# Kernel tuning notes

Measured on AMD Instinct MI355X. Metric: run time of the kernel, lower is better.

Reference implementation:

```python
import jax, jax.numpy as jnp
import numpy as np

B, N, F, H, F_ = 4, 2048, 64, 4, 64


def setup_inputs() -> dict:
    key = jax.random.key(0)
    kx, ka, kw, ks, kn = jax.random.split(key, 5)
    X = jax.random.normal(kx, (B, N, F), dtype=jnp.float32)
    A = (jax.random.uniform(ka, (B, N, N)) < 0.05).astype(jnp.float32)
    A = jnp.maximum(A, jnp.eye(N, dtype=jnp.float32)[None])
    W = jax.random.normal(kw, (H, F, F_), dtype=jnp.float32) * 0.1
    a_self = jax.random.normal(ks, (H, F_), dtype=jnp.float32) * 0.1
    a_neigh = jax.random.normal(kn, (H, F_), dtype=jnp.float32) * 0.1
    return {"X": X, "A": A, "W": W, "a_self": a_self, "a_neigh": a_neigh}


def reference(X, A, W, a_self, a_neigh):
    # linear transform per head: [B,H,N,F_]
    lin = jnp.einsum('bnf,hfo->bhno', X, W)
    # additive attention scores
    s_self = jnp.einsum('bhno,ho->bhn', lin, a_self)[:, :, :, None]   # [B,H,N,1]
    s_neigh = jnp.einsum('bhno,ho->bhn', lin, a_neigh)[:, :, None, :]  # [B,H,1,N]
    dense = s_self + s_neigh                                           # [B,H,N,N]
    dense = jnp.where(dense >= 0, dense, 0.2 * dense)                  # LeakyReLU(0.2)
    BIG = jnp.float32(1e10)
    mask = jnp.exp(A * -BIG) * -BIG                                    # 0 where edge, -1e10 where no edge
    logits = dense + mask[:, None, :, :]
    attn = jax.nn.softmax(logits, axis=-1)
    # dropout is identity at inference (attn_dropout=0.0)
    feats = jnp.einsum('bhnm,bhmo->bhno', attn, lin)                   # [B,H,N,F_]
    feats = jax.nn.relu(feats)                                         # activation before concat
    b, h, n, f_ = feats.shape
    out = feats.transpose(0, 2, 1, 3).reshape(b, n, h * f_)            # concat heads
    return out
```

## Files before the change

### kernel.cpp

```cpp
#include <hip/hip_runtime.h>

#define BB 4
#define NN 2048
#define FF 64
#define HH 4
#define FO 64
#define CAP 256

typedef unsigned short ushort_t;


__global__ __launch_bounds__(256) void BatchGraphAttention_84378927497895_kernel(
    const float* __restrict__ W, const float* __restrict__ a_self,
    const float* __restrict__ a_neigh, float* __restrict__ w_self,
    float* __restrict__ w_neigh) {
  int t = threadIdx.x;
  int h = t >> 6;
  const float* Wp = W + t * FO;
  const float* as = a_self + h * FO;
  const float* an = a_neigh + h * FO;
  float acc_s = 0.f, acc_n = 0.f;
#pragma unroll
  for (int o = 0; o < FO; ++o) {
    float w = Wp[o];
    acc_s += w * as[o];
    acc_n += w * an[o];
  }
  w_self[t] = acc_s;
  w_neigh[t] = acc_n;
}

__global__ __launch_bounds__(256) void BatchGraphAttention_84378927497895_kernel2(
    const float* __restrict__ X, const float* __restrict__ w_self,
    const float* __restrict__ w_neigh, float* __restrict__ s_self4,
    float* __restrict__ s_neigh4) {
  int t = threadIdx.x, lane = t & 63, wv = t >> 6;
  int bn = blockIdx.x * 4 + wv;
  int g = lane & 15;
  int h = lane >> 4;
  float4 x = ((const float4*)X)[(size_t)bn * 16 + g];
  float4 ws = ((const float4*)w_self)[h * 16 + g];
  float4 wn = ((const float4*)w_neigh)[h * 16 + g];
  float vs = x.x * ws.x + x.y * ws.y + x.z * ws.z + x.w * ws.w;
  float vn = x.x * wn.x + x.y * wn.y + x.z * wn.z + x.w * wn.w;
#pragma unroll
  for (int off = 1; off < 16; off <<= 1) {
    vs += __shfl_xor(vs, off, 64);
    vn += __shfl_xor(vn, off, 64);
  }
  if (g == 0) {
    s_self4[bn * 4 + h] = vs;
    s_neigh4[bn * 4 + h] = vn;
  }
}

__global__ __launch_bounds__(256, 8) void BatchGraphAttention_84378927497895_kernel3(
    const float* __restrict__ A, const float* __restrict__ X,
    const float* __restrict__ W, const float* __restrict__ s_self4,
    const float* __restrict__ s_neigh4, float* __restrict__ out) {
  __shared__ float4 plt[4][CAP];
  __shared__ ushort_t idxs[4][CAP];
  int t = threadIdx.x, lane = t & 63, wv = t >> 6;
  int bn = blockIdx.x * 4 + wv;
  int b = bn >> 11;
  float4* pl = plt[wv];
  ushort_t* idx = idxs[wv];

  const float4* Ar = (const float4*)(A + (size_t)bn * NN);
  unsigned long long lt = (1ull << lane) - 1ull;
  int cnt = 0;
#pragma unroll
  for (int r = 0; r < 8; ++r) {
    float4 av = Ar[r * 64 + lane];
    unsigned c = (unsigned)((r * 64 + lane) * 4);
    unsigned long long m0 = __ballot(av.x != 0.f);
    if (av.x != 0.f) { int p = cnt + (int)__popcll(m0 & lt); if (p < CAP) idx[p] = (ushort_t)c; }
    cnt += (int)__popcll(m0);
    unsigned long long m1 = __ballot(av.y != 0.f);
    if (av.y != 0.f) { int p = cnt + (int)__popcll(m1 & lt); if (p < CAP) idx[p] = (ushort_t)(c + 1); }
    cnt += (int)__popcll(m1);
    unsigned long long m2 = __ballot(av.z != 0.f);
    if (av.z != 0.f) { int p = cnt + (int)__popcll(m2 & lt); if (p < CAP) idx[p] = (ushort_t)(c + 2); }
    cnt += (int)__popcll(m2);
    unsigned long long m3 = __ballot(av.w != 0.f);
    if (av.w != 0.f) { int p = cnt + (int)__popcll(m3 & lt); if (p < CAP) idx[p] = (ushort_t)(c + 3); }
    cnt += (int)__popcll(m3);
  }
  cnt = __builtin_amdgcn_readfirstlane(cnt);
  if (cnt > CAP) cnt = CAP;
  int pcnt = (cnt + 7) & ~7;

  float4 ss = ((const float4*)s_self4)[bn];
  const float4* sn = ((const float4*)s_neigh4) + (size_t)b * NN;
  float4 sum = make_float4(0.f, 0.f, 0.f, 0.f);
#define EXP_GAT(K)                                                          \
  {                                                                         \
    int j = lane + K * 64;                                                  \
    if (j < cnt) {                                                          \
      int m = idx[j];                                                       \
      float4 s = sn[m];                                                     \
      float4 lg;                                                            \
      lg.x = ss.x + s.x; lg.y = ss.y + s.y;                                 \
      lg.z = ss.z + s.z; lg.w = ss.w + s.w;                                 \
      lg.x = (lg.x >= 0.f) ? lg.x : 0.2f * lg.x;                            \
      lg.y = (lg.y >= 0.f) ? lg.y : 0.2f * lg.y;                            \
      lg.z = (lg.z >= 0.f) ? lg.z : 0.2f * lg.z;                            \
      lg.w = (lg.w >= 0.f) ? lg.w : 0.2f * lg.w;                            \
      float4 e;                                                             \
      e.x = __expf(lg.x); e.y = __expf(lg.y);                               \
      e.z = __expf(lg.z); e.w = __expf(lg.w);                               \
      sum.x += e.x; sum.y += e.y; sum.z += e.z; sum.w += e.w;               \
      pl[j] = e;                                                            \
    } else if (j < pcnt) {                                                  \
      pl[j] = make_float4(0.f, 0.f, 0.f, 0.f);                              \
      idx[j] = 0;             \
    }                                                                       \
  }
  EXP_GAT(0) EXP_GAT(1) EXP_GAT(2) EXP_GAT(3)
#undef EXP_GAT

  const float* xp = X + (size_t)b * (NN * FF) + lane;
  float y0 = 0.f, y1 = 0.f, y2 = 0.f, y3 = 0.f;
  {
    uint4 pk = *(const uint4*)idx;
    int a0 = pk.x & 0xffff, a1 = pk.x >> 16;
    int a2 = pk.y & 0xffff, a3 = pk.y >> 16;
    int a4 = pk.z & 0xffff, a5 = pk.z >> 16;
    int a6 = pk.w & 0xffff, a7 = pk.w >> 16;
    float xa0 = xp[a0 * FF], xa1 = xp[a1 * FF];
    float xa2 = xp[a2 * FF], xa3 = xp[a3 * FF];
    float xa4 = xp[a4 * FF], xa5 = xp[a5 * FF];
    float xa6 = xp[a6 * FF], xa7 = xp[a7 * FF];
    for (int j = 0; j < pcnt; j += 8) {
      int jn = (j + 8 < pcnt) ? (j + 8) : 0;
      uint4 pn = *(const uint4*)(idx + jn);
      int i0 = pn.x & 0xffff, i1 = pn.x >> 16;
      int i2 = pn.y & 0xffff, i3 = pn.y >> 16;
      int i4 = pn.z & 0xffff, i5 = pn.z >> 16;
      int i6 = pn.w & 0xffff, i7 = pn.w >> 16;
      float xb0 = xp[i0 * FF], xb1 = xp[i1 * FF];
      float xb2 = xp[i2 * FF], xb3 = xp[i3 * FF];
      float xb4 = xp[i4 * FF], xb5 = xp[i5 * FF];
      float xb6 = xp[i6 * FF], xb7 = xp[i7 * FF];
      float4 p0 = pl[j + 0], p1 = pl[j + 1];
      float4 p2 = pl[j + 2], p3 = pl[j + 3];
      y0 += p0.x * xa0; y1 += p0.y * xa0; y2 += p0.z * xa0; y3 += p0.w * xa0;
      y0 += p1.x * xa1; y1 += p1.y * xa1; y2 += p1.z * xa1; y3 += p1.w * xa1;
      y0 += p2.x * xa2; y1 += p2.y * xa2; y2 += p2.z * xa2; y3 += p2.w * xa2;
      y0 += p3.x * xa3; y1 += p3.y * xa3; y2 += p3.z * xa3; y3 += p3.w * xa3;
      float4 p4 = pl[j + 4], p5 = pl[j + 5];
      float4 p6 = pl[j + 6], p7 = pl[j + 7];
      y0 += p4.x * xa4; y1 += p4.y * xa4; y2 += p4.z * xa4; y3 += p4.w * xa4;
      y0 += p5.x * xa5; y1 += p5.y * xa5; y2 += p5.z * xa5; y3 += p5.w * xa5;
      y0 += p6.x * xa6; y1 += p6.y * xa6; y2 += p6.z * xa6; y3 += p6.w * xa6;
      y0 += p7.x * xa7; y1 += p7.y * xa7; y2 += p7.z * xa7; y3 += p7.w * xa7;
      xa0 = xb0; xa1 = xb1; xa2 = xb2; xa3 = xb3;
      xa4 = xb4; xa5 = xb5; xa6 = xb6; xa7 = xb7;
    }
  }

#pragma unroll
  for (int off = 1; off < 64; off <<= 1) {
    sum.x += __shfl_xor(sum.x, off, 64);
    sum.y += __shfl_xor(sum.y, off, 64);
    sum.z += __shfl_xor(sum.z, off, 64);
    sum.w += __shfl_xor(sum.w, off, 64);
  }
  float4 sv;
  sv.x = 1.f / sum.x; sv.y = 1.f / sum.y; sv.z = 1.f / sum.z; sv.w = 1.f / sum.w;

  pl[lane] = make_float4(y0 * sv.x, y1 * sv.y, y2 * sv.z, y3 * sv.w);
  __syncthreads();

  {
    const float* Wh = W + wv * (FF * FO) + lane;
    const float* y0p = (const float*)plt[0] + wv;
    const float* y1p = (const float*)plt[1] + wv;
    const float* y2p = (const float*)plt[2] + wv;
    const float* y3p = (const float*)plt[3] + wv;
    float o0 = 0.f, o1 = 0.f, o2 = 0.f, o3 = 0.f;
#pragma unroll 8
    for (int f = 0; f < FF; ++f) {
      float wl = Wh[f * FO];
      o0 += y0p[f * 4] * wl;
      o1 += y1p[f * 4] * wl;
      o2 += y2p[f * 4] * wl;
      o3 += y3p[f * 4] * wl;
    }
    size_t ob = (size_t)(blockIdx.x * 4) * (HH * FO) + wv * FO + lane;
    out[ob + 0 * (HH * FO)] = fmaxf(o0, 0.f);
    out[ob + 1 * (HH * FO)] = fmaxf(o1, 0.f);
    out[ob + 2 * (HH * FO)] = fmaxf(o2, 0.f);
    out[ob + 3 * (HH * FO)] = fmaxf(o3, 0.f);
  }
}

extern "C" void kernel_launch(void* const* d_in, const int* in_sizes, int n_in,
                              void* d_out, int out_size, void* d_ws,
                              size_t ws_size, hipStream_t stream) {
  const float* X = (const float*)d_in[0];
  const float* A = (const float*)d_in[1];
  const float* W = (const float*)d_in[2];
  const float* a_self = (const float*)d_in[3];
  const float* a_neigh = (const float*)d_in[4];
  float* out = (float*)d_out;

  float* w_self = (float*)d_ws;
  float* w_neigh = w_self + HH * FF;
  float* s_self4 = w_neigh + HH * FF;
  float* s_neigh4 = s_self4 + (size_t)BB * NN * HH;

  BatchGraphAttention_84378927497895_kernel<<<1, 256, 0, stream>>>(
      W, a_self, a_neigh, w_self, w_neigh);
  BatchGraphAttention_84378927497895_kernel2<<<BB * NN / 4, 256, 0, stream>>>(
      X, w_self, w_neigh, s_self4, s_neigh4);
  BatchGraphAttention_84378927497895_kernel3<<<BB * NN / 4, 256, 0, stream>>>(
      A, X, W, s_self4, s_neigh4, out);
}
```

Before: 130.0 us.

## Gather X rows as float4 per quarter-wave and pre-transpose W for float4 projection

The neighbour aggregation loop changes from one scalar X element per lane over eight neighbours to a layout where each quarter-wave handles one neighbour and loads a float4 of X, with cross-quarter shuffles reducing the partial sums. This cuts the number of gather instructions per row and widens the memory accesses. W is also rearranged into a float4-interleaved buffer inside kernel2, so the final per-head projection can use vector loads from both W and shared memory. The costs are extra shuffle reductions and a small transpose step that needs additional workspace.

```diff
diff --git a/kernel.cpp b/kernel.cpp
--- a/kernel.cpp
+++ b/kernel.cpp
@@ -32,7 +32,8 @@
 
 __global__ __launch_bounds__(256) void BatchGraphAttention_84378927497895_kernel2(
     const float* __restrict__ X, const float* __restrict__ w_self,
-    const float* __restrict__ w_neigh, float* __restrict__ s_self4,
+    const float* __restrict__ w_neigh, const float* __restrict__ W,
+    float* __restrict__ WT2, float* __restrict__ s_self4,
     float* __restrict__ s_neigh4) {
   int t = threadIdx.x, lane = t & 63, wv = t >> 6;
   int bn = blockIdx.x * 4 + wv;
@@ -52,11 +53,22 @@
     s_self4[bn * 4 + h] = vs;
     s_neigh4[bn * 4 + h] = vn;
   }
+  if (blockIdx.x < 16) {
+    int gg = blockIdx.x;
+    int hh = t >> 6, o = t & 63;
+    const float* Wb = W + (size_t)(hh * FF) * FO + o;
+    float4 wt;
+    wt.x = Wb[(4 * gg + 0) * FO];
+    wt.y = Wb[(4 * gg + 1) * FO];
+    wt.z = Wb[(4 * gg + 2) * FO];
+    wt.w = Wb[(4 * gg + 3) * FO];
+    ((float4*)WT2)[(hh * 16 + gg) * 64 + o] = wt;
+  }
 }
 
 __global__ __launch_bounds__(256, 8) void BatchGraphAttention_84378927497895_kernel3(
     const float* __restrict__ A, const float* __restrict__ X,
-    const float* __restrict__ W, const float* __restrict__ s_self4,
+    const float* __restrict__ WT2, const float* __restrict__ s_self4,
     const float* __restrict__ s_neigh4, float* __restrict__ out) {
   __shared__ float4 plt[4][CAP];
   __shared__ ushort_t idxs[4][CAP];
@@ -88,7 +100,7 @@
   }
   cnt = __builtin_amdgcn_readfirstlane(cnt);
   if (cnt > CAP) cnt = CAP;
-  int pcnt = (cnt + 7) & ~7;
+  int pcnt = (cnt + 3) & ~3;
 
   float4 ss = ((const float4*)s_self4)[bn];
   const float4* sn = ((const float4*)s_neigh4) + (size_t)b * NN;
@@ -119,45 +131,39 @@
   EXP_GAT(0) EXP_GAT(1) EXP_GAT(2) EXP_GAT(3)
 #undef EXP_GAT
 
-  const float* xp = X + (size_t)b * (NN * FF) + lane;
-  float y0 = 0.f, y1 = 0.f, y2 = 0.f, y3 = 0.f;
+  int q = lane >> 4;
+  int g = lane & 15;
+  const float4* xq = (const float4*)(X + (size_t)b * (NN * FF)) + g;
+  int shamt = (q & 1) * 16;
+  bool hi = (q & 2) != 0;
+  float4 acc0 = make_float4(0.f, 0.f, 0.f, 0.f);
+  float4 acc1 = acc0, acc2 = acc0, acc3 = acc0;
   {
-    uint4 pk = *(const uint4*)idx;
-    int a0 = pk.x & 0xffff, a1 = pk.x >> 16;
-    int a2 = pk.y & 0xffff, a3 = pk.y >> 16;
-    int a4 = pk.z & 0xffff, a5 = pk.z >> 16;
-    int a6 = pk.w & 0xffff, a7 = pk.w >> 16;
-    float xa0 = xp[a0 * FF], xa1 = xp[a1 * FF];
-    float xa2 = xp[a2 * FF], xa3 = xp[a3 * FF];
-    float xa4 = xp[a4 * FF], xa5 = xp[a5 * FF];
-    float xa6 = xp[a6 * FF], xa7 = xp[a7 * FF];
-    for (int j = 0; j < pcnt; j += 8) {
-      int jn = (j + 8 < pcnt) ? (j + 8) : 0;
-      uint4 pn = *(const uint4*)(idx + jn);
-      int i0 = pn.x & 0xffff, i1 = pn.x >> 16;
-      int i2 = pn.y & 0xffff, i3 = pn.y >> 16;
-      int i4 = pn.z & 0xffff, i5 = pn.z >> 16;
-      int i6 = pn.w & 0xffff, i7 = pn.w >> 16;
-      float xb0 = xp[i0 * FF], xb1 = xp[i1 * FF];
-      float xb2 = xp[i2 * FF], xb3 = xp[i3 * FF];
-      float xb4 = xp[i4 * FF], xb5 = xp[i5 * FF];
-      float xb6 = xp[i6 * FF], xb7 = xp[i7 * FF];
-      float4 p0 = pl[j + 0], p1 = pl[j + 1];
-      float4 p2 = pl[j + 2], p3 = pl[j + 3];
-      y0 += p0.x * xa0; y1 += p0.y * xa0; y2 += p0.z * xa0; y3 += p0.w * xa0;
-      y0 += p1.x * xa1; y1 += p1.y * xa1; y2 += p1.z * xa1; y3 += p1.w * xa1;
-      y0 += p2.x * xa2; y1 += p2.y * xa2; y2 += p2.z * xa2; y3 += p2.w * xa2;
-      y0 += p3.x * xa3; y1 += p3.y * xa3; y2 += p3.z * xa3; y3 += p3.w * xa3;
-      float4 p4 = pl[j + 4], p5 = pl[j + 5];
-      float4 p6 = pl[j + 6], p7 = pl[j + 7];
-      y0 += p4.x * xa4; y1 += p4.y * xa4; y2 += p4.z * xa4; y3 += p4.w * xa4;
-      y0 += p5.x * xa5; y1 += p5.y * xa5; y2 += p5.z * xa5; y3 += p5.w * xa5;
-      y0 += p6.x * xa6; y1 += p6.y * xa6; y2 += p6.z * xa6; y3 += p6.w * xa6;
-      y0 += p7.x * xa7; y1 += p7.y * xa7; y2 += p7.z * xa7; y3 += p7.w * xa7;
-      xa0 = xb0; xa1 = xb1; xa2 = xb2; xa3 = xb3;
-      xa4 = xb4; xa5 = xb5; xa6 = xb6; xa7 = xb7;
+    uint2 pk = *(const uint2*)idx;
+    unsigned pw = hi ? pk.y : pk.x;
+    int m = (pw >> shamt) & 0xffff;
+    float4 xv = xq[m * 16];
+    for (int j = 0; j < pcnt; j += 4) {
+      int jn = (j + 4 < pcnt) ? (j + 4) : 0;
+      uint2 pk2 = *(const uint2*)(idx + jn);
+      unsigned pw2 = hi ? pk2.y : pk2.x;
+      int m2 = (pw2 >> shamt) & 0xffff;
+      float4 xv2 = xq[m2 * 16];
+      float4 p = pl[j + q];
+      acc0.x += xv.x * p.x; acc0.y += xv.y * p.x; acc0.z += xv.z * p.x; acc0.w += xv.w * p.x;
+      acc1.x += xv.x * p.y; acc1.y += xv.y * p.y; acc1.z += xv.z * p.y; acc1.w += xv.w * p.y;
+      acc2.x += xv.x * p.z; acc2.y += xv.y * p.z; acc2.z += xv.z * p.z; acc2.w += xv.w * p.z;
+      acc3.x += xv.x * p.w; acc3.y += xv.y * p.w; acc3.z += xv.z * p.w; acc3.w += xv.w * p.w;
+      xv = xv2;
     }
   }
+#define XRED(v)                                                             \
+  v.x += __shfl_xor(v.x, 16, 64); v.y += __shfl_xor(v.y, 16, 64);           \
+  v.z += __shfl_xor(v.z, 16, 64); v.w += __shfl_xor(v.w, 16, 64);           \
+  v.x += __shfl_xor(v.x, 32, 64); v.y += __shfl_xor(v.y, 32, 64);           \
+  v.z += __shfl_xor(v.z, 32, 64); v.w += __shfl_xor(v.w, 32, 64);
+  XRED(acc0) XRED(acc1) XRED(acc2) XRED(acc3)
+#undef XRED
 
 #pragma unroll
   for (int off = 1; off < 64; off <<= 1) {
@@ -169,23 +175,35 @@
   float4 sv;
   sv.x = 1.f / sum.x; sv.y = 1.f / sum.y; sv.z = 1.f / sum.z; sv.w = 1.f / sum.w;
 
-  pl[lane] = make_float4(y0 * sv.x, y1 * sv.y, y2 * sv.z, y3 * sv.w);
+  {
+    float* ysr = (float*)pl;
+    if (lane < 16) {
+      ((float4*)(ysr + 0 * FF))[g] = make_float4(acc0.x * sv.x, acc0.y * sv.x, acc0.z * sv.x, acc0.w * sv.x);
+      ((float4*)(ysr + 1 * FF))[g] = make_float4(acc1.x * sv.y, acc1.y * sv.y, acc1.z * sv.y, acc1.w * sv.y);
+      ((float4*)(ysr + 2 * FF))[g] = make_float4(acc2.x * sv.z, acc2.y * sv.z, acc2.z * sv.z, acc2.w * sv.z);
+      ((float4*)(ysr + 3 * FF))[g] = make_float4(acc3.x * sv.w, acc3.y * sv.w, acc3.z * sv.w, acc3.w * sv.w);
+    }
+  }
   __syncthreads();
 
   {
-    const float* Wh = W + wv * (FF * FO) + lane;
-    const float* y0p = (const float*)plt[0] + wv;
-    const float* y1p = (const float*)plt[1] + wv;
-    const float* y2p = (const float*)plt[2] + wv;
-    const float* y3p = (const float*)plt[3] + wv;
+    const float4* wtp = (const float4*)WT2 + (size_t)(wv * 16) * 64 + lane;
+    const float4* yr0 = (const float4*)((const float*)plt[0] + wv * FF);
+    const float4* yr1 = (const float4*)((const float*)plt[1] + wv * FF);
+    const float4* yr2 = (const float4*)((const float*)plt[2] + wv * FF);
+    const float4* yr3 = (const float4*)((const float*)plt[3] + wv * FF);
     float o0 = 0.f, o1 = 0.f, o2 = 0.f, o3 = 0.f;
-#pragma unroll 8
-    for (int f = 0; f < FF; ++f) {
-      float wl = Wh[f * FO];
-      o0 += y0p[f * 4] * wl;
-      o1 += y1p[f * 4] * wl;
-      o2 += y2p[f * 4] * wl;
-      o3 += y3p[f * 4] * wl;
+#pragma unroll 4
+    for (int gg = 0; gg < 16; ++gg) {
+      float4 wt = wtp[gg * 64];
+      float4 a0 = yr0[gg];
+      float4 a1 = yr1[gg];
+      float4 a2 = yr2[gg];
+      float4 a3 = yr3[gg];
+      o0 += a0.x * wt.x + a0.y * wt.y + a0.z * wt.z + a0.w * wt.w;
+      o1 += a1.x * wt.x + a1.y * wt.y + a1.z * wt.z + a1.w * wt.w;
+      o2 += a2.x * wt.x + a2.y * wt.y + a2.z * wt.z + a2.w * wt.w;
+      o3 += a3.x * wt.x + a3.y * wt.y + a3.z * wt.z + a3.w * wt.w;
     }
     size_t ob = (size_t)(blockIdx.x * 4) * (HH * FO) + wv * FO + lane;
     out[ob + 0 * (HH * FO)] = fmaxf(o0, 0.f);
@@ -209,11 +227,12 @@
   float* w_neigh = w_self + HH * FF;
   float* s_self4 = w_neigh + HH * FF;
   float* s_neigh4 = s_self4 + (size_t)BB * NN * HH;
+  float* WT2 = s_neigh4 + (size_t)BB * NN * HH;
 
   BatchGraphAttention_84378927497895_kernel<<<1, 256, 0, stream>>>(
       W, a_self, a_neigh, w_self, w_neigh);
   BatchGraphAttention_84378927497895_kernel2<<<BB * NN / 4, 256, 0, stream>>>(
-      X, w_self, w_neigh, s_self4, s_neigh4);
+      X, w_self, w_neigh, W, WT2, s_self4, s_neigh4);
   BatchGraphAttention_84378927497895_kernel3<<<BB * NN / 4, 256, 0, stream>>>(
-      A, X, W, s_self4, s_neigh4, out);
-}
+      A, X, WT2, s_self4, s_neigh4, out);
+}
```

Measured after the change: 129.3 us. Within noise of the previous version (-0.6%).
